# Optimization experiments

Measured on AMD Instinct MI355X. Metric: run time of the kernel, lower is better.

Reference implementation:

```python
import jax, jax.numpy as jnp
import numpy as np


def setup_inputs() -> dict:
    key = jax.random.key(0)
    ks = jax.random.split(key, 6)
    E, N, S = 6, 4096, 64
    std_b = (2.0 / (S + S)) ** 0.5
    std_a = (2.0 / (S + S)) ** 0.5
    return {
        "x": jax.random.normal(ks[0], (1, N, S), dtype=jnp.float32),
        "edge_matrix": jax.random.uniform(ks[1], (E, N, N), dtype=jnp.float32),
        "ba": jnp.zeros((S,), dtype=jnp.float32),
        "wz_wr_wh": jax.random.normal(ks[2], (E, S, 3 * S), dtype=jnp.float32) * std_b,
        "uz_ur": jax.random.normal(ks[3], (S, 2 * S), dtype=jnp.float32) * std_b,
        "uh": jax.random.normal(ks[4], (S, S), dtype=jnp.float32) * std_a,
        "iteration": 10,
    }


def reference(x, edge_matrix, ba, wz_wr_wh, uz_ur, uh, iteration):
    # x: [1, N, S]; edge_matrix: [E, N, N]; secondary_size == size branch.
    S = uh.shape[0]
    h = x[0]  # [N, S]

    def step(h, _):
        # activation[e] = edge_matrix[e]^T @ h + ba  -> [E, N, S]
        act = jnp.einsum('ejn,js->ens', edge_matrix, h) + ba
        # per-edge-type GRU projections, summed over edge types -> [N, 3S]
        zrh = jnp.einsum('ens,esk->nk', act, wz_wr_wh)
        wz, wr, wh = zrh[:, :S], zrh[:, S:2 * S], zrh[:, 2 * S:]
        uzr = h @ uz_ur  # [N, 2S]
        z = jax.nn.sigmoid(wz + uzr[:, :S])
        r = jax.nn.sigmoid(wr + uzr[:, S:])
        hh = jnp.tanh(wh + (r * h) @ uh)
        return (1.0 - z) * h + z * hh, None

    h, _ = jax.lax.scan(step, h, None, length=int(iteration))
    return h[None]  # [1, N, S]
```

## Files before the change

### kernel.cpp

```cpp
#include <hip/hip_runtime.h>
#include <cstdint>
#include <cstddef>

#define NN 4096
#define SS 64
#define EE 6
#define BN 64
#define KT 64
#define ITERS 10
#define NSG  128

typedef _Float16 f16x8 __attribute__((ext_vector_type(8)));
typedef float f32x4 __attribute__((ext_vector_type(4)));

__device__ __forceinline__ float sigf(float x) { return 1.0f / (1.0f + __expf(-x)); }

__device__ __forceinline__ size_t cb(int e, int wt, int sg, int q) {
    return ((((size_t)e * (NN / 32) + wt) * NSG + sg) * 4 + q) * 512;
}
__device__ __forceinline__ size_t bidx(int sg, int st, int pl) {
    return (((size_t)sg * 4 + st) * 2 + pl) * 512;
}
__device__ __forceinline__ size_t bslot(int n, int s, int pl) {
    const int sg = n >> 5, jo = n & 31;
    const int lane = ((jo >> 3) << 4) | (s & 15);
    return bidx(sg, s >> 4, pl) + (size_t)lane * 8 + (jo & 7);
}

__global__ __launch_bounds__(256) void k_init(const float* __restrict__ x,
                                              float* __restrict__ h,
                                              _Float16* __restrict__ hTf,
                                              _Float16* __restrict__ hTh,
                                              _Float16* __restrict__ hTl) {
    const int t = threadIdx.x;
    const int n = blockIdx.x * 16 + (t & 15);
    const int c0 = (t >> 4) * 4;
    float4 v = *(const float4*)(x + (size_t)n * SS + c0);
    *(float4*)(h + (size_t)n * SS + c0) = v;
    const float vv[4] = {v.x, v.y, v.z, v.w};
#pragma unroll
    for (int k = 0; k < 4; k++) {
        _Float16 hi = (_Float16)vv[k];
        _Float16 lo = (_Float16)(vv[k] - (float)hi);
        if (hTf) {
            hTf[bslot(n, c0 + k, 0)] = hi;
            hTf[bslot(n, c0 + k, 1)] = lo;
        }
        if (hTh) {
            hTh[(size_t)(c0 + k) * NN + n] = hi;
            hTl[(size_t)(c0 + k) * NN + n] = lo;
        }
    }
}

__global__ __launch_bounds__(128, 4) void k_act_pack(const float* __restrict__ edge,
                                                     const _Float16* __restrict__ hTf,
                                                     float* __restrict__ act_part,
                                                     _Float16* __restrict__ eTf,
                                                     int jtot) {
    const int nt = blockIdx.x;
    const int e  = blockIdx.y;
    const int js = blockIdx.z;
    const int tid = threadIdx.x;
    const int w   = tid >> 6;
    const int lane = tid & 63;
    const int ln = lane & 15;
    const int lk = (lane >> 4) * 8;
    const int wt = nt * 2 + w;
    const int n0 = wt * 32;
    const int jbase = js * jtot;
    const int NSTEP = jtot / 32;
    const int sgbase = js * NSTEP;

    const float* A0 = edge + (size_t)e * NN * NN + (size_t)(jbase + lk) * NN + (n0 + ln);
    const float* A1 = A0 + 16;
    _Float16* stbase = eTf + cb(e, wt, sgbase, 0) + (size_t)lane * 8;

    f32x4 acc[2][4];
#pragma unroll
    for (int nh = 0; nh < 2; nh++)
#pragma unroll
        for (int st = 0; st < 4; st++) acc[nh][st] = (f32x4)0.0f;

    f16x8 h0[2], l0[2], h1[2], l1[2];

#define LOADA(H, L, s_)                                                      \
    {                                                                        \
        const int sc = ((s_) < NSTEP) ? (s_) : 0;                            \
        const size_t off = (size_t)sc * 32 * NN;                             \
        float t0[8], t1[8];                                                  \
        _Pragma("unroll")                                                    \
        for (int i = 0; i < 8; i++) {                                        \
            t0[i] = A0[off + (size_t)i * NN];                                \
            t1[i] = A1[off + (size_t)i * NN];                                \
        }                                                                    \
        _Pragma("unroll")                                                    \
        for (int i = 0; i < 8; i++) {                                        \
            _Float16 hi0 = (_Float16)t0[i];                                  \
            H[0][i] = hi0;                                                   \
            L[0][i] = (_Float16)(t0[i] - (float)hi0);                        \
            _Float16 hi1 = (_Float16)t1[i];                                  \
            H[1][i] = hi1;                                                   \
            L[1][i] = (_Float16)(t1[i] - (float)hi1);                        \
        }                                                                    \
        _Float16* sp = stbase + (size_t)sc * 2048;                           \
        *(f16x8*)(sp)        = H[0];                                         \
        *(f16x8*)(sp + 512)  = L[0];                                         \
        *(f16x8*)(sp + 1024) = H[1];                                         \
        *(f16x8*)(sp + 1536) = L[1];                                         \
    }

#define COMPUTE(H, L, s)                                                     \
    {                                                                        \
        f16x8 bh[4], bl[4];                                                  \
        _Pragma("unroll")                                                    \
        for (int st = 0; st < 4; st++) {                                     \
            bh[st] = *(const f16x8*)(hTf + bidx(sgbase + (s), st, 0) + (size_t)lane * 8); \
            bl[st] = *(const f16x8*)(hTf + bidx(sgbase + (s), st, 1) + (size_t)lane * 8); \
        }                                                                    \
        _Pragma("unroll")                                                    \
        for (int nh = 0; nh < 2; nh++) {                                     \
            _Pragma("unroll")                                                \
            for (int st = 0; st < 4; st++) {                                 \
                acc[nh][st] = __builtin_amdgcn_mfma_f32_16x16x32_f16(        \
                    H[nh], bh[st], acc[nh][st], 0, 0, 0);                    \
                acc[nh][st] = __builtin_amdgcn_mfma_f32_16x16x32_f16(        \
                    H[nh], bl[st], acc[nh][st], 0, 0, 0);                    \
                acc[nh][st] = __builtin_amdgcn_mfma_f32_16x16x32_f16(        \
                    L[nh], bh[st], acc[nh][st], 0, 0, 0);                    \
            }                                                                \
        }                                                                    \
    }

    LOADA(h0, l0, 0);
    LOADA(h1, l1, 1);
    for (int s = 0; s < NSTEP; s += 2) {
        COMPUTE(h0, l0, s);     LOADA(h0, l0, s + 2);
        COMPUTE(h1, l1, s + 1); LOADA(h1, l1, s + 3);
    }
#undef LOADA
#undef COMPUTE

    float* ap = act_part + (size_t)(js * EE + e) * NN * SS;
#pragma unroll
    for (int nh = 0; nh < 2; nh++)
#pragma unroll
        for (int st = 0; st < 4; st++)
#pragma unroll
            for (int r = 0; r < 4; r++) {
                const int n = n0 + nh * 16 + (lane >> 4) * 4 + r;
                ap[(size_t)n * SS + st * 16 + ln] = acc[nh][st][r];
            }
}

__global__ __launch_bounds__(64, 4) void k_act4(const _Float16* __restrict__ eTf,
                                                const _Float16* __restrict__ hTf,
                                                float* __restrict__ act_part,
                                                int jtot) {
    const int wt = blockIdx.x;
    const int e  = blockIdx.y;
    const int js = blockIdx.z;
    const int lane = threadIdx.x;
    const int ln = lane & 15;
    const int n0 = wt * 32;
    const int NSTEP = jtot / 32;
    const int sgbase = js * NSTEP;

    const _Float16* Abase = eTf + cb(e, wt, sgbase, 0) + (size_t)lane * 8;

    f32x4 acc[2][4];
#pragma unroll
    for (int nh = 0; nh < 2; nh++)
#pragma unroll
        for (int st = 0; st < 4; st++) acc[nh][st] = (f32x4)0.0f;

    f16x8 H0[2], L0[2], H1[2], L1[2];

#define LOADA(H, L, s_)                                                      \
    {                                                                        \
        const int sc = ((s_) < NSTEP) ? (s_) : 0;                            \
        const _Float16* p = Abase + (size_t)sc * 2048;                       \
        H[0] = *(const f16x8*)(p);                                           \
        L[0] = *(const f16x8*)(p + 512);                                     \
        H[1] = *(const f16x8*)(p + 1024);                                    \
        L[1] = *(const f16x8*)(p + 1536);                                    \
    }

#define COMPUTE(H, L, s)                                                     \
    {                                                                        \
        f16x8 bh[4], bl[4];                                                  \
        _Pragma("unroll")                                                    \
        for (int st = 0; st < 4; st++) {                                     \
            bh[st] = *(const f16x8*)(hTf + bidx(sgbase + (s), st, 0) + (size_t)lane * 8); \
            bl[st] = *(const f16x8*)(hTf + bidx(sgbase + (s), st, 1) + (size_t)lane * 8); \
        }                                                                    \
        _Pragma("unroll")                                                    \
        for (int nh = 0; nh < 2; nh++) {                                     \
            _Pragma("unroll")                                                \
            for (int st = 0; st < 4; st++) {                                 \
                acc[nh][st] = __builtin_amdgcn_mfma_f32_16x16x32_f16(        \
                    H[nh], bh[st], acc[nh][st], 0, 0, 0);                    \
                acc[nh][st] = __builtin_amdgcn_mfma_f32_16x16x32_f16(        \
                    H[nh], bl[st], acc[nh][st], 0, 0, 0);                    \
                acc[nh][st] = __builtin_amdgcn_mfma_f32_16x16x32_f16(        \
                    L[nh], bh[st], acc[nh][st], 0, 0, 0);                    \
            }                                                                \
        }                                                                    \
    }

    LOADA(H0, L0, 0);
    LOADA(H1, L1, 1);
    for (int s = 0; s < NSTEP; s += 2) {
        COMPUTE(H0, L0, s);     LOADA(H0, L0, s + 2);
        COMPUTE(H1, L1, s + 1); LOADA(H1, L1, s + 3);
    }
#undef LOADA
#undef COMPUTE

    float* ap = act_part + (size_t)(js * EE + e) * NN * SS;
#pragma unroll
    for (int nh = 0; nh < 2; nh++)
#pragma unroll
        for (int st = 0; st < 4; st++)
#pragma unroll
            for (int r = 0; r < 4; r++) {
                const int n = n0 + nh * 16 + (lane >> 4) * 4 + r;
                ap[(size_t)n * SS + st * 16 + ln] = acc[nh][st][r];
            }
}

__global__ __launch_bounds__(128, 4) void k_act_mfma(const float* __restrict__ edge,
                                                     const _Float16* __restrict__ hTh,
                                                     const _Float16* __restrict__ hTl,
                                                     float* __restrict__ act_part,
                                                     int jtot) {
    const int nt = blockIdx.x;
    const int e  = blockIdx.y;
    const int js = blockIdx.z;
    const int tid = threadIdx.x;
    const int w   = tid >> 6;
    const int lane = tid & 63;
    const int ln = lane & 15;
    const int lk = (lane >> 4) * 8;
    const int n0 = nt * 64 + w * 32;
    const int jbase = js * jtot;
    const int NSTEP = jtot / 32;

    const float* A0 = edge + (size_t)e * NN * NN + (size_t)(jbase + lk) * NN + (n0 + ln);
    const float* A1 = A0 + 16;
    const size_t bbase = (size_t)ln * NN + jbase + lk;

    f32x4 acc[2][4];
#pragma unroll
    for (int nh = 0; nh < 2; nh++)
#pragma unroll
        for (int st = 0; st < 4; st++) acc[nh][st] = (f32x4)0.0f;

    f16x8 h0[2], l0[2], h1[2], l1[2];

#define LOADA(H, L, s_)                                                      \
    {                                                                        \
        const int sc = ((s_) < NSTEP) ? (s_) : 0;                            \
        const size_t off = (size_t)sc * 32 * NN;                             \
        float t0[8], t1[8];                                                  \
        _Pragma("unroll")                                                    \
        for (int i = 0; i < 8; i++) {                                        \
            t0[i] = A0[off + (size_t)i * NN];                                \
            t1[i] = A1[off + (size_t)i * NN];                                \
        }                                                                    \
        _Pragma("unroll")                                                    \
        for (int i = 0; i < 8; i++) {                                        \
            _Float16 hi0 = (_Float16)t0[i];                                  \
            H[0][i] = hi0;                                                   \
            L[0][i] = (_Float16)(t0[i] - (float)hi0);                        \
            _Float16 hi1 = (_Float16)t1[i];                                  \
            H[1][i] = hi1;                                                   \
            L[1][i] = (_Float16)(t1[i] - (float)hi1);                        \
        }                                                                    \
    }

#define COMPUTE(H, L, s)                                                     \
    {                                                                        \
        f16x8 bh[4], bl[4];                                                  \
        _Pragma("unroll")                                                    \
        for (int st = 0; st < 4; st++) {                                     \
            const size_t bo = bbase + (size_t)st * 16 * NN + (size_t)(s) * 32;\
            bh[st] = *(const f16x8*)(hTh + bo);                              \
            bl[st] = *(const f16x8*)(hTl + bo);                              \
        }                                                                    \
        _Pragma("unroll")                                                    \
        for (int nh = 0; nh < 2; nh++) {                                     \
            _Pragma("unroll")                                                \
            for (int st = 0; st < 4; st++) {                                 \
                acc[nh][st] = __builtin_amdgcn_mfma_f32_16x16x32_f16(        \
                    H[nh], bh[st], acc[nh][st], 0, 0, 0);                    \
                acc[nh][st] = __builtin_amdgcn_mfma_f32_16x16x32_f16(        \
                    H[nh], bl[st], acc[nh][st], 0, 0, 0);                    \
                acc[nh][st] = __builtin_amdgcn_mfma_f32_16x16x32_f16(        \
                    L[nh], bh[st], acc[nh][st], 0, 0, 0);                    \
            }                                                                \
        }                                                                    \
    }

    LOADA(h0, l0, 0);
    LOADA(h1, l1, 1);
    for (int s = 0; s < NSTEP; s += 2) {
        COMPUTE(h0, l0, s);     LOADA(h0, l0, s + 2);
        COMPUTE(h1, l1, s + 1); LOADA(h1, l1, s + 3);
    }
#undef LOADA
#undef COMPUTE

    float* ap = act_part + (size_t)(js * EE + e) * NN * SS;
#pragma unroll
    for (int nh = 0; nh < 2; nh++)
#pragma unroll
        for (int st = 0; st < 4; st++)
#pragma unroll
            for (int r = 0; r < 4; r++) {
                const int n = n0 + nh * 16 + (lane >> 4) * 4 + r;
                ap[(size_t)n * SS + st * 16 + ln] = acc[nh][st][r];
            }
}

__global__ __launch_bounds__(128) void k_act(const float* __restrict__ edge,
                                             const float* __restrict__ h,
                                             float* __restrict__ act_part,
                                             int jtot) {
    __shared__ float hbuf[2][KT][SS];
    const int nb = blockIdx.x;
    const int e  = blockIdx.y;
    const int js = blockIdx.z;
    const int tid = threadIdx.x;
    const int ng = tid & 7;
    const int sg = tid >> 3;
    const int n0 = nb * BN;
    const int s0 = sg * 4;
    const int jbase = js * jtot;

    const float4* hsrc4 = (const float4*)(h + (size_t)jbase * SS);

    float acc[8][4];
#pragma unroll
    for (int i = 0; i < 8; i++)
#pragma unroll
        for (int k = 0; k < 4; k++) acc[i][k] = 0.0f;

    float4 pre[8];
#pragma unroll
    for (int r = 0; r < 8; r++) pre[r] = hsrc4[r * 128 + tid];
    {
        float4* dst = (float4*)&hbuf[0][0][0];
#pragma unroll
        for (int r = 0; r < 8; r++) dst[r * 128 + tid] = pre[r];
    }
    __syncthreads();

    const float* eg = edge + (size_t)e * NN * NN + (size_t)jbase * NN + n0 + ng * 8;

    float4 ea[4][2];
#pragma unroll
    for (int u = 0; u < 4; u++) {
        ea[u][0] = *(const float4*)(eg + (size_t)u * NN);
        ea[u][1] = *(const float4*)(eg + (size_t)u * NN + 4);
    }

    const int NCH = jtot / KT;
    for (int c = 0; c < NCH; c++) {
        if (c + 1 < NCH) {
#pragma unroll
            for (int r = 0; r < 8; r++) pre[r] = hsrc4[(c + 1) * (KT * SS / 4) + r * 128 + tid];
        }
        const float (*hb)[SS] = hbuf[c & 1];
        for (int jj = 0; jj < KT; jj += 4) {
            const int q = c * KT + jj + 4;
            const float* pe = eg + (size_t)(q < jtot ? q : 0) * NN;
            float4 eb[4][2];
#pragma unroll
            for (int u = 0; u < 4; u++) {
                eb[u][0] = *(const float4*)(pe + (size_t)u * NN);
                eb[u][1] = *(const float4*)(pe + (size_t)u * NN + 4);
            }
#pragma unroll
            for (int u = 0; u < 4; u++) {
                const float4 hv = *(const float4*)&hb[jj + u][s0];
                const float ev[8] = {ea[u][0].x, ea[u][0].y, ea[u][0].z, ea[u][0].w,
                                     ea[u][1].x, ea[u][1].y, ea[u][1].z, ea[u][1].w};
#pragma unroll
                for (int i = 0; i < 8; i++) {
                    acc[i][0] += ev[i] * hv.x;
                    acc[i][1] += ev[i] * hv.y;
                    acc[i][2] += ev[i] * hv.z;
                    acc[i][3] += ev[i] * hv.w;
                }
            }
#pragma unroll
            for (int u = 0; u < 4; u++) { ea[u][0] = eb[u][0]; ea[u][1] = eb[u][1]; }
        }
        if (c + 1 < NCH) {
            float4* dst = (float4*)&hbuf[(c + 1) & 1][0][0];
#pragma unroll
            for (int r = 0; r < 8; r++) dst[r * 128 + tid] = pre[r];
        }
        __syncthreads();
    }

    float* ap = act_part + (((size_t)js * EE + e) * NN + n0 + ng * 8) * SS + s0;
#pragma unroll
    for (int i = 0; i < 8; i++)
        *(float4*)(ap + (size_t)i * SS) = make_float4(acc[i][0], acc[i][1], acc[i][2], acc[i][3]);
}

__global__ __launch_bounds__(256) void k_update(const float* __restrict__ act_part,
                                                float* __restrict__ h,
                                                const float* __restrict__ W,
                                                const float* __restrict__ uz_ur,
                                                const float* __restrict__ uh,
                                                const float* __restrict__ ba,
                                                _Float16* __restrict__ hTf,
                                                _Float16* __restrict__ hTh,
                                                _Float16* __restrict__ hTl,
                                                int jparts) {
    __shared__ float w_lds[SS][192];
    __shared__ float a_lds[16][68];
    __shared__ float h_lds[16][68];
    __shared__ float zrh_lds[16][196];
    __shared__ float uzr_lds[16][132];
    __shared__ float rh_lds[16][68];

    const int n0 = blockIdx.x * 16;
    const int t = threadIdx.x;
    const int nl = t & 15;
    const int kg = t >> 4;

    {
        const int row = t >> 4, c4 = t & 15;
        float4 v = *(const float4*)(h + (size_t)(n0 + row) * SS + c4 * 4);
        *(float4*)&h_lds[row][c4 * 4] = v;
    }

    float zacc[12];
#pragma unroll
    for (int k = 0; k < 12; k++) zacc[k] = 0.0f;
    const int k0 = kg * 12;

    for (int e = 0; e < EE; e++) {
        __syncthreads();
        {
            const float4* wsrc = (const float4*)(W + (size_t)e * SS * 192);
            float4* wdst = (float4*)&w_lds[0][0];
#pragma unroll
            for (int r = 0; r < 12; r++) wdst[r * 256 + t] = wsrc[r * 256 + t];
        }
        {
            const int row = t >> 4, c4 = t & 15;
            const size_t base = ((size_t)e * NN + (n0 + row)) * SS + c4 * 4;
            float4 bv = *(const float4*)(ba + c4 * 4);
            float vx = bv.x, vy = bv.y, vz = bv.z, vw = bv.w;
            for (int p = 0; p < jparts; p++) {
                float4 pp = *(const float4*)(act_part + base + (size_t)p * EE * NN * SS);
                vx += pp.x; vy += pp.y; vz += pp.z; vw += pp.w;
            }
            *(float4*)&a_lds[row][c4 * 4] = make_float4(vx, vy, vz, vw);
        }
        __syncthreads();
#pragma unroll 8
        for (int s = 0; s < SS; s++) {
            const float av = a_lds[nl][s];
            const float4* wrow = (const float4*)&w_lds[s][k0];
            const float4 w0 = wrow[0], w1 = wrow[1], w2 = wrow[2];
            zacc[0] += av * w0.x; zacc[1] += av * w0.y; zacc[2]  += av * w0.z; zacc[3]  += av * w0.w;
            zacc[4] += av * w1.x; zacc[5] += av * w1.y; zacc[6]  += av * w1.z; zacc[7]  += av * w1.w;
            zacc[8] += av * w2.x; zacc[9] += av * w2.y; zacc[10] += av * w2.z; zacc[11] += av * w2.w;
        }
    }

    float uacc[8];
#pragma unroll
    for (int k = 0; k < 8; k++) uacc[k] = 0.0f;
#pragma unroll 4
    for (int j = 0; j < SS; j++) {
        const float hv = h_lds[nl][j];
        const float4* urow = (const float4*)(uz_ur + (size_t)j * 128 + kg * 8);
        const float4 u0 = urow[0], u1 = urow[1];
        uacc[0] += hv * u0.x; uacc[1] += hv * u0.y; uacc[2] += hv * u0.z; uacc[3] += hv * u0.w;
        uacc[4] += hv * u1.x; uacc[5] += hv * u1.y; uacc[6] += hv * u1.z; uacc[7] += hv * u1.w;
    }

    *(float4*)&zrh_lds[nl][k0]     = make_float4(zacc[0], zacc[1], zacc[2], zacc[3]);
    *(float4*)&zrh_lds[nl][k0 + 4] = make_float4(zacc[4], zacc[5], zacc[6], zacc[7]);
    *(float4*)&zrh_lds[nl][k0 + 8] = make_float4(zacc[8], zacc[9], zacc[10], zacc[11]);
    *(float4*)&uzr_lds[nl][kg * 8]     = make_float4(uacc[0], uacc[1], uacc[2], uacc[3]);
    *(float4*)&uzr_lds[nl][kg * 8 + 4] = make_float4(uacc[4], uacc[5], uacc[6], uacc[7]);
    __syncthreads();

    const int sg4 = kg * 4;
    const float4 wz = *(const float4*)&zrh_lds[nl][sg4];
    const float4 wr = *(const float4*)&zrh_lds[nl][64 + sg4];
    const float4 wh = *(const float4*)&zrh_lds[nl][128 + sg4];
    const float4 uz = *(const float4*)&uzr_lds[nl][sg4];
    const float4 ur = *(const float4*)&uzr_lds[nl][64 + sg4];
    const float4 hv4 = *(const float4*)&h_lds[nl][sg4];

    float z4[4], rh4[4];
    {
        const float wzv[4] = {wz.x, wz.y, wz.z, wz.w};
        const float wrv[4] = {wr.x, wr.y, wr.z, wr.w};
        const float uzv[4] = {uz.x, uz.y, uz.z, uz.w};
        const float urv[4] = {ur.x, ur.y, ur.z, ur.w};
        const float hvv[4] = {hv4.x, hv4.y, hv4.z, hv4.w};
#pragma unroll
        for (int k = 0; k < 4; k++) {
            z4[k] = sigf(wzv[k] + uzv[k]);
            const float r = sigf(wrv[k] + urv[k]);
            rh4[k] = r * hvv[k];
        }
    }
    *(float4*)&rh_lds[nl][sg4] = make_float4(rh4[0], rh4[1], rh4[2], rh4[3]);
    __syncthreads();

    float hacc[4];
#pragma unroll
    for (int k = 0; k < 4; k++) hacc[k] = 0.0f;
#pragma unroll 4
    for (int j = 0; j < SS; j++) {
        const float rhv = rh_lds[nl][j];
        const float4 u = *(const float4*)(uh + (size_t)j * SS + sg4);
        hacc[0] += rhv * u.x; hacc[1] += rhv * u.y; hacc[2] += rhv * u.z; hacc[3] += rhv * u.w;
    }

    {
        const float whv[4] = {wh.x, wh.y, wh.z, wh.w};
        const float hvv[4] = {hv4.x, hv4.y, hv4.z, hv4.w};
        float ov[4];
#pragma unroll
        for (int k = 0; k < 4; k++) {
            const float hh = tanhf(whv[k] + hacc[k]);
            ov[k] = (1.0f - z4[k]) * hvv[k] + z4[k] * hh;
        }
        const int n = n0 + nl;
        *(float4*)(h + (size_t)n * SS + sg4) = make_float4(ov[0], ov[1], ov[2], ov[3]);
#pragma unroll
        for (int k = 0; k < 4; k++) {
            _Float16 hi = (_Float16)ov[k];
            _Float16 lo = (_Float16)(ov[k] - (float)hi);
            if (hTf) {
                hTf[bslot(n, sg4 + k, 0)] = hi;
                hTf[bslot(n, sg4 + k, 1)] = lo;
            }
            if (hTh) {
                hTh[(size_t)(sg4 + k) * NN + n] = hi;
                hTl[(size_t)(sg4 + k) * NN + n] = lo;
            }
        }
    }
}

extern "C" void kernel_launch(void* const* d_in, const int* in_sizes, int n_in,
                              void* d_out, int out_size, void* d_ws, size_t ws_size,
                              hipStream_t stream) {
    const float* x    = (const float*)d_in[0];
    const float* edge = (const float*)d_in[1];
    const float* ba   = (const float*)d_in[2];
    const float* W    = (const float*)d_in[3];
    const float* uzur = (const float*)d_in[4];
    const float* uh   = (const float*)d_in[5];

    float* h = (float*)d_out;
    char*  wsb = (char*)d_ws;

    const size_t actB = (size_t)EE * NN * SS * sizeof(float);
    const size_t hTfB = (size_t)NSG * 4 * 2 * 512 * sizeof(_Float16);
    const size_t hTBu = (size_t)SS * NN * sizeof(_Float16) * 2;
    const size_t eTfB = (size_t)EE * NN * NN * 2 * sizeof(_Float16);
    const int jp = 4;
    const size_t needFull = eTfB + (size_t)jp * actB + hTfB;

    if (ws_size >= needFull) {
        _Float16* eTf = (_Float16*)wsb;
        float*    act = (float*)(wsb + eTfB);
        _Float16* hTf = (_Float16*)(wsb + eTfB + (size_t)jp * actB);
        const int jtot = NN / jp;

        k_init<<<NN / 16, 256, 0, stream>>>(x, h, hTf, nullptr, nullptr);

        k_act_pack<<<dim3(NN / 64, EE, jp), 128, 0, stream>>>(edge, hTf, act, eTf, jtot);
        k_update<<<NN / 16, 256, 0, stream>>>(act, h, W, uzur, uh, ba, hTf, nullptr, nullptr, jp);

        for (int it = 1; it < ITERS; ++it) {
            k_act4<<<dim3(NN / 32, EE, jp), 64, 0, stream>>>(eTf, hTf, act, jtot);
            k_update<<<NN / 16, 256, 0, stream>>>(act, h, W, uzur, uh, ba, hTf, nullptr, nullptr, jp);
        }
    } else {
        int jp2;
        bool use_mfma;
        if      (ws_size >= 4 * actB + hTBu) { jp2 = 4; use_mfma = true;  }
        else if (ws_size >= 2 * actB + hTBu) { jp2 = 2; use_mfma = true;  }
        else if (ws_size >= 1 * actB + hTBu) { jp2 = 1; use_mfma = true;  }
        else                                 { jp2 = 1; use_mfma = false; }

        float*     act = (float*)wsb;
        _Float16*  hTh = use_mfma ? (_Float16*)(wsb + (size_t)jp2 * actB) : nullptr;
        _Float16*  hTl = use_mfma ? (_Float16*)(wsb + (size_t)jp2 * actB) + (size_t)SS * NN : nullptr;
        const int jtot = NN / jp2;

        k_init<<<NN / 16, 256, 0, stream>>>(x, h, nullptr, hTh, hTl);
        for (int it = 0; it < ITERS; ++it) {
            if (use_mfma) {
                k_act_mfma<<<dim3(NN / 64, EE, jp2), 128, 0, stream>>>(edge, hTh, hTl, act, jtot);
            } else {
                k_act<<<dim3(NN / BN, EE, jp2), 128, 0, stream>>>(edge, h, act, jtot);
            }
            k_update<<<NN / 16, 256, 0, stream>>>(act, h, W, uzur, uh, ba, nullptr, hTh, hTl, jp2);
        }
    }
}
```

Measured before the change: 1.489 ms.

## Stage edge-matrix tiles through LDS with coalesced float4 loads

The first-pass kernel used to load the edge matrix with strided scalar loads, one row element per lane, which produced poorly coalesced global reads. It now reads 32x32 tiles with float4 loads, eight lanes per row, into a padded per-wave LDS double buffer. Each lane then reads its transposed fragment from LDS, splits it into fp16 hi/lo, stores the packed copy and feeds the MFMAs. No barriers are used between the LDS writes and reads. That is only safe because each wave owns its own buffer and runs in lockstep, and it costs extra LDS traffic and a larger shared-memory footprint per block.

After: 1.518 ms. About the same (+2.0%).

```diff
diff --git a/kernel.cpp b/kernel.cpp
--- a/kernel.cpp
+++ b/kernel.cpp
@@ -58,6 +58,7 @@
                                                      float* __restrict__ act_part,
                                                      _Float16* __restrict__ eTf,
                                                      int jtot) {
+    __shared__ float tile_s[2][2][32][33];
     const int nt = blockIdx.x;
     const int e  = blockIdx.y;
     const int js = blockIdx.z;
@@ -72,8 +73,11 @@
     const int NSTEP = jtot / 32;
     const int sgbase = js * NSTEP;
 
-    const float* A0 = edge + (size_t)e * NN * NN + (size_t)(jbase + lk) * NN + (n0 + ln);
-    const float* A1 = A0 + 16;
+    const int gr = lane >> 3;
+    const int gc = (lane & 7) * 4;
+    const float* eb = edge + (size_t)e * NN * NN + (size_t)jbase * NN + n0 + gc;
+    float (*tl)[32][33] = tile_s[w];
+
     _Float16* stbase = eTf + cb(e, wt, sgbase, 0) + (size_t)lane * 8;
 
     f32x4 acc[2][4];
@@ -82,36 +86,46 @@
 #pragma unroll
         for (int st = 0; st < 4; st++) acc[nh][st] = (f32x4)0.0f;
 
-    f16x8 h0[2], l0[2], h1[2], l1[2];
-
-#define LOADA(H, L, s_)                                                      \
+    float4 pre[4];
+
+#define LOADG(s_)                                                            \
     {                                                                        \
         const int sc = ((s_) < NSTEP) ? (s_) : 0;                            \
-        const size_t off = (size_t)sc * 32 * NN;                             \
-        float t0[8], t1[8];                                                  \
+        _Pragma("unroll")                                                    \
+        for (int q = 0; q < 4; q++)                                          \
+            pre[q] = *(const float4*)(eb + (size_t)(sc * 32 + gr + 8 * q) * NN); \
+    }
+
+#define WRITELDS(b)                                                          \
+    {                                                                        \
+        _Pragma("unroll")                                                    \
+        for (int q = 0; q < 4; q++) {                                        \
+            const float pv[4] = {pre[q].x, pre[q].y, pre[q].z, pre[q].w};    \
+            _Pragma("unroll")                                                \
+            for (int k = 0; k < 4; k++)                                      \
+                tl[b][gr + 8 * q][gc + k] = pv[k];                           \
+        }                                                                    \
+    }
+
+#define COMPUTE(b, s)                                                        \
+    {                                                                        \
+        f16x8 H[2], L[2];                                                    \
         _Pragma("unroll")                                                    \
         for (int i = 0; i < 8; i++) {                                        \
-            t0[i] = A0[off + (size_t)i * NN];                                \
-            t1[i] = A1[off + (size_t)i * NN];                                \
-        }                                                                    \
-        _Pragma("unroll")                                                    \
-        for (int i = 0; i < 8; i++) {                                        \
-            _Float16 hi0 = (_Float16)t0[i];                                  \
+            const float v0 = tl[b][lk + i][ln];                              \
+            const float v1 = tl[b][lk + i][ln + 16];                         \
+            _Float16 hi0 = (_Float16)v0;                                     \
             H[0][i] = hi0;                                                   \
-            L[0][i] = (_Float16)(t0[i] - (float)hi0);                        \
-            _Float16 hi1 = (_Float16)t1[i];                                  \
+            L[0][i] = (_Float16)(v0 - (float)hi0);                           \
+            _Float16 hi1 = (_Float16)v1;                                     \
             H[1][i] = hi1;                                                   \
-            L[1][i] = (_Float16)(t1[i] - (float)hi1);                        \
-        }                                                                    \
-        _Float16* sp = stbase + (size_t)sc * 2048;                           \
+            L[1][i] = (_Float16)(v1 - (float)hi1);                           \
+        }                                                                    \
+        _Float16* sp = stbase + (size_t)(s) * 2048;                          \
         *(f16x8*)(sp)        = H[0];                                         \
         *(f16x8*)(sp + 512)  = L[0];                                         \
         *(f16x8*)(sp + 1024) = H[1];                                         \
         *(f16x8*)(sp + 1536) = L[1];                                         \
-    }
-
-#define COMPUTE(H, L, s)                                                     \
-    {                                                                        \
         f16x8 bh[4], bl[4];                                                  \
         _Pragma("unroll")                                                    \
         for (int st = 0; st < 4; st++) {                                     \
@@ -132,13 +146,19 @@
         }                                                                    \
     }
 
-    LOADA(h0, l0, 0);
-    LOADA(h1, l1, 1);
+    LOADG(0);
+    WRITELDS(0);
+    LOADG(1);
     for (int s = 0; s < NSTEP; s += 2) {
-        COMPUTE(h0, l0, s);     LOADA(h0, l0, s + 2);
-        COMPUTE(h1, l1, s + 1); LOADA(h1, l1, s + 3);
-    }
-#undef LOADA
+        WRITELDS(1);
+        LOADG(s + 2);
+        COMPUTE(0, s);
+        WRITELDS(0);
+        LOADG(s + 3);
+        COMPUTE(1, s + 1);
+    }
+#undef LOADG
+#undef WRITELDS
 #undef COMPUTE
 
     float* ap = act_part + (size_t)(js * EE + e) * NN * SS;
```

## Split act4 work per 16-row half-tile with matching packed-edge layout

Applied to the files above, without the earlier changes.

Changes the packed fp16 hi/lo edge layout so each 16-row half of a 32-row tile is contiguous, and replaces k_act4 with k_act4n, where each single-wave block handles only 16 output rows. This doubles the grid size and halves per-wave accumulators and registers, with launch bounds raised to six blocks per unit for more occupancy and latency hiding. In exchange, each block re-reads the same B (hT) fragments, so B-side traffic doubles.

Result: slower. 1.739 ms (+16.8%).

```diff
diff --git a/kernel.cpp b/kernel.cpp
--- a/kernel.cpp
+++ b/kernel.cpp
@@ -15,8 +15,8 @@
 
 __device__ __forceinline__ float sigf(float x) { return 1.0f / (1.0f + __expf(-x)); }
 
-__device__ __forceinline__ size_t cb(int e, int wt, int sg, int q) {
-    return ((((size_t)e * (NN / 32) + wt) * NSG + sg) * 4 + q) * 512;
+__device__ __forceinline__ size_t cb2(int e, int wt, int nh, int sg, int pl) {
+    return (((((size_t)e * (NN / 32) + wt) * 2 + nh) * NSG + sg) * 2 + pl) * 512;
 }
 __device__ __forceinline__ size_t bidx(int sg, int st, int pl) {
     return (((size_t)sg * 4 + st) * 2 + pl) * 512;
@@ -74,7 +74,8 @@
 
     const float* A0 = edge + (size_t)e * NN * NN + (size_t)(jbase + lk) * NN + (n0 + ln);
     const float* A1 = A0 + 16;
-    _Float16* stbase = eTf + cb(e, wt, sgbase, 0) + (size_t)lane * 8;
+    _Float16* stb0 = eTf + cb2(e, wt, 0, sgbase, 0) + (size_t)lane * 8;
+    _Float16* stb1 = eTf + cb2(e, wt, 1, sgbase, 0) + (size_t)lane * 8;
 
     f32x4 acc[2][4];
 #pragma unroll
@@ -103,11 +104,12 @@
             H[1][i] = hi1;                                                   \
             L[1][i] = (_Float16)(t1[i] - (float)hi1);                        \
         }                                                                    \
-        _Float16* sp = stbase + (size_t)sc * 2048;                           \
-        *(f16x8*)(sp)        = H[0];                                         \
-        *(f16x8*)(sp + 512)  = L[0];                                         \
-        *(f16x8*)(sp + 1024) = H[1];                                         \
-        *(f16x8*)(sp + 1536) = L[1];                                         \
+        _Float16* sp0 = stb0 + (size_t)sc * 1024;                            \
+        *(f16x8*)(sp0)       = H[0];                                         \
+        *(f16x8*)(sp0 + 512) = L[0];                                         \
+        _Float16* sp1 = stb1 + (size_t)sc * 1024;                            \
+        *(f16x8*)(sp1)       = H[1];                                         \
+        *(f16x8*)(sp1 + 512) = L[1];                                         \
     }
 
 #define COMPUTE(H, L, s)                                                     \
@@ -153,37 +155,35 @@
             }
 }
 
-__global__ __launch_bounds__(64, 4) void k_act4(const _Float16* __restrict__ eTf,
-                                                const _Float16* __restrict__ hTf,
-                                                float* __restrict__ act_part,
-                                                int jtot) {
-    const int wt = blockIdx.x;
+__global__ __launch_bounds__(64, 6) void k_act4n(const _Float16* __restrict__ eTf,
+                                                 const _Float16* __restrict__ hTf,
+                                                 float* __restrict__ act_part,
+                                                 int jtot) {
+    const int bx = blockIdx.x;
     const int e  = blockIdx.y;
     const int js = blockIdx.z;
+    const int wt = bx >> 1;
+    const int nh = bx & 1;
     const int lane = threadIdx.x;
     const int ln = lane & 15;
-    const int n0 = wt * 32;
+    const int n0 = bx * 16;
     const int NSTEP = jtot / 32;
     const int sgbase = js * NSTEP;
 
-    const _Float16* Abase = eTf + cb(e, wt, sgbase, 0) + (size_t)lane * 8;
-
-    f32x4 acc[2][4];
-#pragma unroll
-    for (int nh = 0; nh < 2; nh++)
-#pragma unroll
-        for (int st = 0; st < 4; st++) acc[nh][st] = (f32x4)0.0f;
-
-    f16x8 H0[2], L0[2], H1[2], L1[2];
+    const _Float16* Abase = eTf + cb2(e, wt, nh, sgbase, 0) + (size_t)lane * 8;
+
+    f32x4 acc[4];
+#pragma unroll
+    for (int st = 0; st < 4; st++) acc[st] = (f32x4)0.0f;
+
+    f16x8 H0, L0, H1, L1;
 
 #define LOADA(H, L, s_)                                                      \
     {                                                                        \
         const int sc = ((s_) < NSTEP) ? (s_) : 0;                            \
-        const _Float16* p = Abase + (size_t)sc * 2048;                       \
-        H[0] = *(const f16x8*)(p);                                           \
-        L[0] = *(const f16x8*)(p + 512);                                     \
-        H[1] = *(const f16x8*)(p + 1024);                                    \
-        L[1] = *(const f16x8*)(p + 1536);                                    \
+        const _Float16* p = Abase + (size_t)sc * 1024;                       \
+        H = *(const f16x8*)(p);                                              \
+        L = *(const f16x8*)(p + 512);                                        \
     }
 
 #define COMPUTE(H, L, s)                                                     \
@@ -195,16 +195,13 @@
             bl[st] = *(const f16x8*)(hTf + bidx(sgbase + (s), st, 1) + (size_t)lane * 8); \
         }                                                                    \
         _Pragma("unroll")                                                    \
-        for (int nh = 0; nh < 2; nh++) {                                     \
-            _Pragma("unroll")                                                \
-            for (int st = 0; st < 4; st++) {                                 \
-                acc[nh][st] = __builtin_amdgcn_mfma_f32_16x16x32_f16(        \
-                    H[nh], bh[st], acc[nh][st], 0, 0, 0);                    \
-                acc[nh][st] = __builtin_amdgcn_mfma_f32_16x16x32_f16(        \
-                    H[nh], bl[st], acc[nh][st], 0, 0, 0);                    \
-                acc[nh][st] = __builtin_amdgcn_mfma_f32_16x16x32_f16(        \
-                    L[nh], bh[st], acc[nh][st], 0, 0, 0);                    \
-            }                                                                \
+        for (int st = 0; st < 4; st++) {                                     \
+            acc[st] = __builtin_amdgcn_mfma_f32_16x16x32_f16(                \
+                H, bh[st], acc[st], 0, 0, 0);                                \
+            acc[st] = __builtin_amdgcn_mfma_f32_16x16x32_f16(                \
+                H, bl[st], acc[st], 0, 0, 0);                                \
+            acc[st] = __builtin_amdgcn_mfma_f32_16x16x32_f16(                \
+                L, bh[st], acc[st], 0, 0, 0);                                \
         }                                                                    \
     }
 
@@ -219,14 +216,12 @@
 
     float* ap = act_part + (size_t)(js * EE + e) * NN * SS;
 #pragma unroll
-    for (int nh = 0; nh < 2; nh++)
-#pragma unroll
-        for (int st = 0; st < 4; st++)
-#pragma unroll
-            for (int r = 0; r < 4; r++) {
-                const int n = n0 + nh * 16 + (lane >> 4) * 4 + r;
-                ap[(size_t)n * SS + st * 16 + ln] = acc[nh][st][r];
-            }
+    for (int st = 0; st < 4; st++)
+#pragma unroll
+        for (int r = 0; r < 4; r++) {
+            const int n = n0 + (lane >> 4) * 4 + r;
+            ap[(size_t)n * SS + st * 16 + ln] = acc[st][r];
+        }
 }
 
 __global__ __launch_bounds__(128, 4) void k_act_mfma(const float* __restrict__ edge,
@@ -588,7 +583,7 @@
         k_update<<<NN / 16, 256, 0, stream>>>(act, h, W, uzur, uh, ba, hTf, nullptr, nullptr, jp);
 
         for (int it = 1; it < ITERS; ++it) {
-            k_act4<<<dim3(NN / 32, EE, jp), 64, 0, stream>>>(eTf, hTf, act, jtot);
+            k_act4n<<<dim3(NN / 16, EE, jp), 64, 0, stream>>>(eTf, hTf, act, jtot);
             k_update<<<NN / 16, 256, 0, stream>>>(act, h, W, uzur, uh, ba, hTf, nullptr, nullptr, jp);
         }
     } else {
```
